# Optimization experiments

Hardware: AMD Instinct MI355X
Metric: run time of the kernel (lower is better)

Reference implementation:

```python
import jax, jax.numpy as jnp
import numpy as np

N_NODES = 100000
H_FEATS = 256
N_EDGES = 300000
NUM_CLASSES = 1


def setup_inputs() -> dict:
    key = jax.random.key(0)
    k1, k2, k3, k4, k5 = jax.random.split(key, 5)
    x = jax.random.normal(k1, (N_NODES, H_FEATS), dtype=jnp.float32)
    edge_index = jax.random.randint(k2, (2, N_EDGES), 0, N_NODES, dtype=jnp.int64)
    # MLP params (stored as [in, out] for x @ W + b)
    in1 = 2 * H_FEATS
    W1 = jax.random.normal(k3, (in1, H_FEATS), dtype=jnp.float32) / np.sqrt(in1)
    b1 = jnp.zeros((H_FEATS,), dtype=jnp.float32)
    W2 = jax.random.normal(k4, (H_FEATS, NUM_CLASSES), dtype=jnp.float32) / np.sqrt(H_FEATS)
    b2 = jnp.zeros((NUM_CLASSES,), dtype=jnp.float32)
    return {"x": x, "edge_index": edge_index, "W1": W1, "b1": b1, "W2": W2, "b2": b2}


def reference(x, edge_index, W1, b1, W2, b2):
    # Gather source/dest node embeddings and concat -> [E, 2*h_feats]
    h = jnp.concatenate([x[edge_index[0]], x[edge_index[1]]], axis=-1)
    h = jax.nn.relu(h @ W1 + b1)          # [E, h_feats]
    h = h @ W2 + b2                        # [E, num_classes]
    return jnp.squeeze(h, axis=1)          # [E]
```

## Files before the change

### kernel.cpp

```cpp
#include <hip/hip_runtime.h>
#include <hip/hip_bf16.h>

#define NN 100000
#define H  256
#define NE 300000
#define KOUT 512
#define MT  782

typedef __attribute__((ext_vector_type(8))) short short8;
typedef __attribute__((ext_vector_type(8))) unsigned short ushort8v;
typedef __attribute__((ext_vector_type(4))) float f32x4;

__device__ __forceinline__ unsigned short f2bf(float f) {
    unsigned int u = __float_as_uint(f);
    u += 0x7FFFu + ((u >> 16) & 1u);
    return (unsigned short)(u >> 16);
}
__device__ __forceinline__ float bf2f(unsigned short h) {
    return __uint_as_float(((unsigned int)h) << 16);
}
__device__ __forceinline__ int swz(int row, int coloff) {
    return row * 128 + (coloff ^ ((row & 7) << 4));
}
__device__ __forceinline__ void gload16(const void* g, void* l) {
    __builtin_amdgcn_global_load_lds((const __attribute__((address_space(1))) void*)g,
                                     (__attribute__((address_space(3))) void*)l,
                                     16, 0, 0);
}

__global__ __launch_bounds__(256) void wprep(const float* __restrict__ W1,
                                             unsigned short* __restrict__ wsB) {
    int gtid = blockIdx.x * 256 + threadIdx.x;
    int t  = gtid >> 10;
    int kg = (gtid >> 7) & 7;
    int n  = gtid & 127;
    int nt = t >> 2, ks = t & 3;
    int krow0 = ks * 64 + kg * 8 + ((nt >= 2) ? 256 : 0);
    int col = (nt & 1) * 128 + n;
    const float* src = W1 + (size_t)krow0 * 256 + col;
    ushort8v p;
    #pragma unroll
    for (int i = 0; i < 8; ++i) p[i] = f2bf(src[(size_t)i * 256]);
    *(ushort8v*)((char*)(wsB + t * 8192) + swz(n, kg * 16)) = p;
}

__global__ __launch_bounds__(512) void xprep2(const float* __restrict__ x,
                                              unsigned short* __restrict__ xb) {
    int gid = blockIdx.x * 512 + threadIdx.x;
    int t   = gid >> 9;
    int rem = gid & 511;
    int r   = rem >> 2;
    int gp  = (rem & 3) * 2;
    int mt = t >> 2, ks = t & 3;
    int node = mt * 128 + r; if (node > NN - 1) node = NN - 1;
    const float* src = x + (size_t)node * H + ks * 64 + gp * 8;
    float4 v0 = *(const float4*)(src);
    float4 v1 = *(const float4*)(src + 4);
    float4 v2 = *(const float4*)(src + 8);
    float4 v3 = *(const float4*)(src + 12);
    ushort8v p0, p1;
    p0[0]=f2bf(v0.x); p0[1]=f2bf(v0.y); p0[2]=f2bf(v0.z); p0[3]=f2bf(v0.w);
    p0[4]=f2bf(v1.x); p0[5]=f2bf(v1.y); p0[6]=f2bf(v1.z); p0[7]=f2bf(v1.w);
    p1[0]=f2bf(v2.x); p1[1]=f2bf(v2.y); p1[2]=f2bf(v2.z); p1[3]=f2bf(v2.w);
    p1[4]=f2bf(v3.x); p1[5]=f2bf(v3.y); p1[6]=f2bf(v3.z); p1[7]=f2bf(v3.w);
    char* dst = (char*)(xb + (size_t)t * 8192);
    *(ushort8v*)(dst + swz(r, gp * 16))      = p0;
    *(ushort8v*)(dst + swz(r, gp * 16 + 16)) = p1;
}

__global__ __launch_bounds__(256) void gemm_v8(const unsigned short* __restrict__ xb,
                                               const unsigned short* __restrict__ wsB,
                                               unsigned short* __restrict__ y) {
    __shared__ unsigned short Al[2][8192];
    __shared__ unsigned short Bl[2][8192];
    const int tid = threadIdx.x;
    const int logical = ((int)blockIdx.x & 7) * ((int)gridDim.x >> 3) + ((int)blockIdx.x >> 3);
    const int mt = logical >> 2, nt = logical & 3;
    const int m0 = mt * 128, n0 = nt * 128;
    const int lane = tid & 63, wid = tid >> 6;
    const int wm = (wid >> 1) * 64, wn = (wid & 1) * 64;
    const int lr = lane & 15, lk = lane >> 4;

    const char* asrc = (const char*)(xb + (size_t)mt * 4 * 8192) + wid * 4096 + lane * 16;
    const char* bsrc = (const char*)(wsB + nt * 4 * 8192) + wid * 4096 + lane * 16;

    f32x4 acc[4][4] = {};

    #pragma unroll
    for (int i = 0; i < 4; ++i) {
        gload16(asrc + i * 1024, (char*)Al[0] + wid * 4096 + i * 1024);
        gload16(bsrc + i * 1024, (char*)Bl[0] + wid * 4096 + i * 1024);
    }
    __syncthreads();

    #pragma unroll
    for (int ks = 0; ks < 4; ++ks) {
        if (ks < 3) {
            const int nb = (ks + 1) & 1;
            #pragma unroll
            for (int i = 0; i < 4; ++i) {
                gload16(asrc + (ks + 1) * 16384 + i * 1024, (char*)Al[nb] + wid * 4096 + i * 1024);
                gload16(bsrc + (ks + 1) * 16384 + i * 1024, (char*)Bl[nb] + wid * 4096 + i * 1024);
            }
        }
        const char* Ab = (const char*)Al[ks & 1];
        const char* Bb = (const char*)Bl[ks & 1];
        #pragma unroll
        for (int kk = 0; kk < 64; kk += 32) {
            const int coloff = kk * 2 + lk * 16;
            short8 a[4], b[4];
            #pragma unroll
            for (int mi = 0; mi < 4; ++mi)
                a[mi] = *(const short8*)(Ab + swz(wm + mi * 16 + lr, coloff));
            #pragma unroll
            for (int ni = 0; ni < 4; ++ni)
                b[ni] = *(const short8*)(Bb + swz(wn + ni * 16 + lr, coloff));
            #pragma unroll
            for (int ni = 0; ni < 4; ++ni)
                #pragma unroll
                for (int mi = 0; mi < 4; ++mi)
                    acc[ni][mi] = __builtin_amdgcn_mfma_f32_16x16x32_bf16(b[ni], a[mi], acc[ni][mi], 0, 0, 0);
        }
        __syncthreads();
    }
    #pragma unroll
    for (int mi = 0; mi < 4; ++mi) {
        const int node = m0 + wm + mi * 16 + lr;
        if (node < NN) {
            #pragma unroll
            for (int ni = 0; ni < 4; ++ni) {
                const int feat = n0 + wn + ni * 16 + lk * 4;
                ushort4 u;
                u.x = f2bf(acc[ni][mi][0]);
                u.y = f2bf(acc[ni][mi][1]);
                u.z = f2bf(acc[ni][mi][2]);
                u.w = f2bf(acc[ni][mi][3]);
                *(ushort4*)(y + (size_t)node * KOUT + feat) = u;
            }
        }
    }
}

__global__ __launch_bounds__(256) void edge_v2(const unsigned short* __restrict__ y,
                                               const int* __restrict__ ei,
                                               const float* __restrict__ b1,
                                               const float* __restrict__ W2,
                                               const float* __restrict__ b2,
                                               float* __restrict__ out) {
    const int tid = threadIdx.x;
    const int l32 = tid & 31;
    const int ghw = ((int)(blockIdx.x * blockDim.x) + tid) >> 5;
    const int nhw = ((int)(gridDim.x * blockDim.x)) >> 5;
    const int j = l32 * 8;
    const float4 b01 = *(const float4*)(b1 + j);
    const float4 b23 = *(const float4*)(b1 + j + 4);
    const float4 w01 = *(const float4*)(W2 + j);
    const float4 w23 = *(const float4*)(W2 + j + 4);
    const float bb = b2[0];
    #pragma unroll 2
    for (int e = ghw; e < NE; e += nhw) {
        int s = ei[e], d = ei[NE + e];
        s = s < 0 ? 0 : (s > NN - 1 ? NN - 1 : s);
        d = d < 0 ? 0 : (d > NN - 1 ? NN - 1 : d);
        ushort8v us = *(const ushort8v*)(y + (size_t)s * KOUT + j);
        ushort8v ud = *(const ushort8v*)(y + (size_t)d * KOUT + 256 + j);
        float acc;
        acc  = fmaxf(bf2f(us[0]) + bf2f(ud[0]) + b01.x, 0.f) * w01.x;
        acc += fmaxf(bf2f(us[1]) + bf2f(ud[1]) + b01.y, 0.f) * w01.y;
        acc += fmaxf(bf2f(us[2]) + bf2f(ud[2]) + b01.z, 0.f) * w01.z;
        acc += fmaxf(bf2f(us[3]) + bf2f(ud[3]) + b01.w, 0.f) * w01.w;
        acc += fmaxf(bf2f(us[4]) + bf2f(ud[4]) + b23.x, 0.f) * w23.x;
        acc += fmaxf(bf2f(us[5]) + bf2f(ud[5]) + b23.y, 0.f) * w23.y;
        acc += fmaxf(bf2f(us[6]) + bf2f(ud[6]) + b23.z, 0.f) * w23.z;
        acc += fmaxf(bf2f(us[7]) + bf2f(ud[7]) + b23.w, 0.f) * w23.w;
        #pragma unroll
        for (int off = 16; off > 0; off >>= 1) acc += __shfl_xor(acc, off, 64);
        if (l32 == 0) out[e] = acc + bb;
    }
}

__global__ __launch_bounds__(256) void fused_fallback(const float* __restrict__ x,
                                                      const int* __restrict__ ei,
                                                      const float* __restrict__ W1,
                                                      const float* __restrict__ b1,
                                                      const float* __restrict__ W2,
                                                      const float* __restrict__ b2,
                                                      float* __restrict__ out) {
    __shared__ float xsh[4][512];
    const int lane = threadIdx.x & 63;
    const int wl = threadIdx.x >> 6;
    const int gw = (blockIdx.x * blockDim.x + threadIdx.x) >> 6;
    const int nw = (gridDim.x * blockDim.x) >> 6;
    const int j = lane * 4;
    const float4 bv = *(const float4*)(b1 + j);
    const float4 wv = *(const float4*)(W2 + j);
    const float bb = b2[0];
    for (int e = gw; e < NE; e += nw) {
        int s = ei[e], d = ei[NE + e];
        s = min(max(s, 0), NN - 1);
        d = min(max(d, 0), NN - 1);
        __threadfence_block();
        #pragma unroll
        for (int i = 0; i < 4; ++i) {
            xsh[wl][i * 64 + lane]       = x[(size_t)s * H + i * 64 + lane];
            xsh[wl][256 + i * 64 + lane] = x[(size_t)d * H + i * 64 + lane];
        }
        __threadfence_block();
        float h0 = bv.x, h1 = bv.y, h2 = bv.z, h3 = bv.w;
        for (int k = 0; k < 256; ++k) {
            float xa = xsh[wl][k], xb2 = xsh[wl][256 + k];
            float4 wa = *(const float4*)(W1 + (size_t)k * 256 + j);
            float4 wb = *(const float4*)(W1 + (size_t)(k + 256) * 256 + j);
            h0 += xa * wa.x + xb2 * wb.x;
            h1 += xa * wa.y + xb2 * wb.y;
            h2 += xa * wa.z + xb2 * wb.z;
            h3 += xa * wa.w + xb2 * wb.w;
        }
        float acc = fmaxf(h0, 0.f) * wv.x + fmaxf(h1, 0.f) * wv.y +
                    fmaxf(h2, 0.f) * wv.z + fmaxf(h3, 0.f) * wv.w;
        #pragma unroll
        for (int off = 32; off > 0; off >>= 1) acc += __shfl_xor(acc, off, 64);
        if (lane == 0) out[e] = acc + bb;
    }
}

extern "C" void kernel_launch(void* const* d_in, const int* in_sizes, int n_in,
                              void* d_out, int out_size, void* d_ws, size_t ws_size,
                              hipStream_t stream) {
    const float* x  = (const float*)d_in[0];
    const int*   ei = (const int*)d_in[1];
    const float* W1 = (const float*)d_in[2];
    const float* b1 = (const float*)d_in[3];
    const float* W2 = (const float*)d_in[4];
    const float* b2 = (const float*)d_in[5];
    float* out = (float*)d_out;

    const size_t ybytes  = (size_t)NN * KOUT * sizeof(unsigned short);
    const size_t xbbytes = (size_t)MT * 4 * 16384;
    const size_t wbytes  = 16 * 8192 * sizeof(unsigned short);

    if (ws_size >= ybytes + xbbytes + wbytes) {
        unsigned short* yb  = (unsigned short*)d_ws;
        unsigned short* xbb = (unsigned short*)((char*)d_ws + ybytes);
        unsigned short* wb  = (unsigned short*)((char*)d_ws + ybytes + xbbytes);
        wprep<<<dim3(64), dim3(256), 0, stream>>>(W1, wb);
        xprep2<<<dim3(MT * 4), dim3(512), 0, stream>>>(x, xbb);
        gemm_v8<<<dim3(MT * 4), dim3(256), 0, stream>>>(xbb, wb, yb);
        edge_v2<<<dim3(2048), dim3(256), 0, stream>>>(yb, ei, b1, W2, b2, out);
    } else {
        fused_fallback<<<dim3(2048), dim3(256), 0, stream>>>(x, ei, W1, b1, W2, b2, out);
    }
}
```

Baseline: 135.4 us.

## Read A operand directly from row-major bf16 x, dropping LDS staging

The x-to-bf16 conversion now writes a plain row-major layout through a grid-stride loop instead of a swizzled tiled layout. The GEMM kernel loads A fragments straight from global memory into registers rather than staging them in LDS, which halves shared memory use and allows an occupancy hint of 4 blocks per SM. The last barrier is skipped. This removes the LDS traffic for A but makes each A fragment an uncoalesced 16-byte global read per lane, with no prefetch to hide its latency.

After: 154.6 us. 14.2% more time.

```diff
diff --git a/kernel.cpp b/kernel.cpp
--- a/kernel.cpp
+++ b/kernel.cpp
@@ -44,34 +44,23 @@
     *(ushort8v*)((char*)(wsB + t * 8192) + swz(n, kg * 16)) = p;
 }
 
-__global__ __launch_bounds__(512) void xprep2(const float* __restrict__ x,
+__global__ __launch_bounds__(256) void xprep3(const float* __restrict__ x,
                                               unsigned short* __restrict__ xb) {
-    int gid = blockIdx.x * 512 + threadIdx.x;
-    int t   = gid >> 9;
-    int rem = gid & 511;
-    int r   = rem >> 2;
-    int gp  = (rem & 3) * 2;
-    int mt = t >> 2, ks = t & 3;
-    int node = mt * 128 + r; if (node > NN - 1) node = NN - 1;
-    const float* src = x + (size_t)node * H + ks * 64 + gp * 8;
-    float4 v0 = *(const float4*)(src);
-    float4 v1 = *(const float4*)(src + 4);
-    float4 v2 = *(const float4*)(src + 8);
-    float4 v3 = *(const float4*)(src + 12);
-    ushort8v p0, p1;
-    p0[0]=f2bf(v0.x); p0[1]=f2bf(v0.y); p0[2]=f2bf(v0.z); p0[3]=f2bf(v0.w);
-    p0[4]=f2bf(v1.x); p0[5]=f2bf(v1.y); p0[6]=f2bf(v1.z); p0[7]=f2bf(v1.w);
-    p1[0]=f2bf(v2.x); p1[1]=f2bf(v2.y); p1[2]=f2bf(v2.z); p1[3]=f2bf(v2.w);
-    p1[4]=f2bf(v3.x); p1[5]=f2bf(v3.y); p1[6]=f2bf(v3.z); p1[7]=f2bf(v3.w);
-    char* dst = (char*)(xb + (size_t)t * 8192);
-    *(ushort8v*)(dst + swz(r, gp * 16))      = p0;
-    *(ushort8v*)(dst + swz(r, gp * 16 + 16)) = p1;
-}
-
-__global__ __launch_bounds__(256) void gemm_v8(const unsigned short* __restrict__ xb,
-                                               const unsigned short* __restrict__ wsB,
-                                               unsigned short* __restrict__ y) {
-    __shared__ unsigned short Al[2][8192];
+    const int total = NN * H / 8;
+    for (int g = blockIdx.x * 256 + threadIdx.x; g < total; g += gridDim.x * 256) {
+        const float* s = x + (size_t)g * 8;
+        float4 v0 = *(const float4*)(s);
+        float4 v1 = *(const float4*)(s + 4);
+        ushort8v p;
+        p[0]=f2bf(v0.x); p[1]=f2bf(v0.y); p[2]=f2bf(v0.z); p[3]=f2bf(v0.w);
+        p[4]=f2bf(v1.x); p[5]=f2bf(v1.y); p[6]=f2bf(v1.z); p[7]=f2bf(v1.w);
+        *(ushort8v*)(xb + (size_t)g * 8) = p;
+    }
+}
+
+__global__ __launch_bounds__(256, 4) void gemm_v9(const unsigned short* __restrict__ xb,
+                                                  const unsigned short* __restrict__ wsB,
+                                                  unsigned short* __restrict__ y) {
     __shared__ unsigned short Bl[2][8192];
     const int tid = threadIdx.x;
     const int logical = ((int)blockIdx.x & 7) * ((int)gridDim.x >> 3) + ((int)blockIdx.x >> 3);
@@ -81,29 +70,30 @@
     const int wm = (wid >> 1) * 64, wn = (wid & 1) * 64;
     const int lr = lane & 15, lk = lane >> 4;
 
-    const char* asrc = (const char*)(xb + (size_t)mt * 4 * 8192) + wid * 4096 + lane * 16;
+    const unsigned short* arow[4];
+    #pragma unroll
+    for (int mi = 0; mi < 4; ++mi) {
+        int node = m0 + wm + mi * 16 + lr;
+        if (node > NN - 1) node = NN - 1;
+        arow[mi] = xb + (size_t)node * H + lk * 8;
+    }
     const char* bsrc = (const char*)(wsB + nt * 4 * 8192) + wid * 4096 + lane * 16;
 
     f32x4 acc[4][4] = {};
 
     #pragma unroll
-    for (int i = 0; i < 4; ++i) {
-        gload16(asrc + i * 1024, (char*)Al[0] + wid * 4096 + i * 1024);
+    for (int i = 0; i < 4; ++i)
         gload16(bsrc + i * 1024, (char*)Bl[0] + wid * 4096 + i * 1024);
-    }
     __syncthreads();
 
     #pragma unroll
     for (int ks = 0; ks < 4; ++ks) {
         if (ks < 3) {
-            const int nb = (ks + 1) & 1;
-            #pragma unroll
-            for (int i = 0; i < 4; ++i) {
-                gload16(asrc + (ks + 1) * 16384 + i * 1024, (char*)Al[nb] + wid * 4096 + i * 1024);
-                gload16(bsrc + (ks + 1) * 16384 + i * 1024, (char*)Bl[nb] + wid * 4096 + i * 1024);
-            }
-        }
-        const char* Ab = (const char*)Al[ks & 1];
+            #pragma unroll
+            for (int i = 0; i < 4; ++i)
+                gload16(bsrc + (ks + 1) * 16384 + i * 1024,
+                        (char*)Bl[(ks + 1) & 1] + wid * 4096 + i * 1024);
+        }
         const char* Bb = (const char*)Bl[ks & 1];
         #pragma unroll
         for (int kk = 0; kk < 64; kk += 32) {
@@ -111,7 +101,7 @@
             short8 a[4], b[4];
             #pragma unroll
             for (int mi = 0; mi < 4; ++mi)
-                a[mi] = *(const short8*)(Ab + swz(wm + mi * 16 + lr, coloff));
+                a[mi] = *(const short8*)(arow[mi] + ks * 64 + kk);
             #pragma unroll
             for (int ni = 0; ni < 4; ++ni)
                 b[ni] = *(const short8*)(Bb + swz(wn + ni * 16 + lr, coloff));
@@ -121,7 +111,7 @@
                 for (int mi = 0; mi < 4; ++mi)
                     acc[ni][mi] = __builtin_amdgcn_mfma_f32_16x16x32_bf16(b[ni], a[mi], acc[ni][mi], 0, 0, 0);
         }
-        __syncthreads();
+        if (ks < 3) __syncthreads();
     }
     #pragma unroll
     for (int mi = 0; mi < 4; ++mi) {
@@ -236,7 +226,7 @@
     float* out = (float*)d_out;
 
     const size_t ybytes  = (size_t)NN * KOUT * sizeof(unsigned short);
-    const size_t xbbytes = (size_t)MT * 4 * 16384;
+    const size_t xbbytes = (size_t)NN * H * sizeof(unsigned short);
     const size_t wbytes  = 16 * 8192 * sizeof(unsigned short);
 
     if (ws_size >= ybytes + xbbytes + wbytes) {
@@ -244,8 +234,8 @@
         unsigned short* xbb = (unsigned short*)((char*)d_ws + ybytes);
         unsigned short* wb  = (unsigned short*)((char*)d_ws + ybytes + xbbytes);
         wprep<<<dim3(64), dim3(256), 0, stream>>>(W1, wb);
-        xprep2<<<dim3(MT * 4), dim3(512), 0, stream>>>(x, xbb);
-        gemm_v8<<<dim3(MT * 4), dim3(256), 0, stream>>>(xbb, wb, yb);
+        xprep3<<<dim3(2048), dim3(256), 0, stream>>>(x, xbb);
+        gemm_v9<<<dim3(MT * 4), dim3(256), 0, stream>>>(xbb, wb, yb);
         edge_v2<<<dim3(2048), dim3(256), 0, stream>>>(yb, ei, b1, W2, b2, out);
     } else {
         fused_fallback<<<dim3(2048), dim3(256), 0, stream>>>(x, ei, W1, b1, W2, b2, out);
```
